# Performance work log

Measured on AMD Instinct MI355X. Metric: run time of the kernel, lower is better.

The kernel has to match this reference:

```python
import jax, jax.numpy as jnp
import numpy as np

B, M, N, DIM = 4, 3, 2048, 512
H = 4
HD = DIM // H  # 128
SCALE = float(np.sqrt(HD))  # code divides scores by sqrt(head_dim)


def setup_inputs() -> dict:
    key = jax.random.key(0)
    ks = jax.random.split(key, 9)
    s = 0.02
    return {
        "query": jax.random.normal(ks[0], (B, M, N, DIM), jnp.float32),
        "key": jax.random.normal(ks[1], (B, M, N, DIM), jnp.float32),
        "value": jax.random.normal(ks[2], (B, M, N, DIM), jnp.float32),
        "Wq": jax.random.normal(ks[3], (DIM, DIM), jnp.float32) * s,
        "bq": jax.random.normal(ks[4], (DIM,), jnp.float32) * s,
        "Wk": jax.random.normal(ks[5], (DIM, DIM), jnp.float32) * s,
        "bk": jax.random.normal(ks[6], (DIM,), jnp.float32) * s,
        "Wv": jax.random.normal(ks[7], (DIM, DIM), jnp.float32) * s,
        "bv": jax.random.normal(ks[8], (DIM,), jnp.float32) * s,
    }


def reference(query, key, value, Wq, bq, Wk, bk, Wv, bv):
    b, m, n, dim = query.shape
    # nn.Linear: x @ W.T + b
    Q = (query @ Wq.T + bq).reshape(b, m, n, H, HD)
    K = (key @ Wk.T + bk).reshape(b, m, n, H, HD)
    V = (value @ Wv.T + bv).reshape(b, m, n, H, HD)
    # scores: [b, m, H, n, n]
    scores = jnp.einsum("bmqhd,bmkhd->bmhqk", Q, K) / SCALE
    attn = jax.nn.softmax(scores, axis=-1)
    out = jnp.einsum("bmhqk,bmkhd->bmqhd", attn, V)
    return out.reshape(b, m, n, dim)
```

## Files before the change

kernel.cpp:

```cpp
#include <hip/hip_runtime.h>
#include <hip/hip_bf16.h>


typedef short s16x8 __attribute__((ext_vector_type(8)));
typedef unsigned short u16x8 __attribute__((ext_vector_type(8)));
typedef float f32x4 __attribute__((ext_vector_type(4)));

#define MFMA16(a, b, c) __builtin_amdgcn_mfma_f32_16x16x32_bf16((a), (b), (c), 0, 0, 0)

static __device__ __forceinline__ unsigned short f2bf(float f) {
    union { float f; unsigned u; } v; v.f = f;
    unsigned r = v.u + 0x7FFFu + ((v.u >> 16) & 1u);
    return (unsigned short)(r >> 16);
}
static __device__ __forceinline__ unsigned pk2(float a, float b) {
    unsigned r;
    asm("v_cvt_pk_bf16_f32 %0, %1, %2" : "=v"(r) : "v"(a), "v"(b));
    return r;
}
static __device__ __forceinline__ float exp2_hw(float x) {
    float r;
    asm("v_exp_f32 %0, %1" : "=v"(r) : "v"(x));
    return r;
}

#define CEXP_F 0.12755102905911087f

#define OSTR 72

__global__ __launch_bounds__(256, 2)
void qkv_proj_kernel(const float* __restrict__ Xq, const float* __restrict__ Xk,
                     const float* __restrict__ Xv,
                     const float* __restrict__ Wq, const float* __restrict__ bq,
                     const float* __restrict__ Wk, const float* __restrict__ bk,
                     const float* __restrict__ Wv, const float* __restrict__ bv,
                     unsigned short* __restrict__ ws_q,
                     unsigned short* __restrict__ ws_k,
                     unsigned short* __restrict__ ws_vt)
{
    __shared__ __align__(16) char smem[65536];

    const int which = blockIdx.z;
    const float* X    = (which == 0) ? Xq : (which == 1) ? Xk : Xv;
    const float* W    = (which == 0) ? Wq : (which == 1) ? Wk : Wv;
    const float* bias = (which == 0) ? bq : (which == 1) ? bk : bv;

    const int r0 = blockIdx.x * 128;
    const int c0 = blockIdx.y * 128;
    const int tid = threadIdx.x;
    const int lane = tid & 63, wave = tid >> 6;
    const int l15 = lane & 15, quad = lane >> 4;
    const int wr = (wave >> 1) * 64, wc = (wave & 1) * 64;

    const int srow = tid >> 4;
    const int scol = tid & 15;
    const int cf = scol * 4;
    const int cb = scol * 8;

    f32x4 acc[4][4] = {};

    {
        char* A0 = smem;
        char* B0 = smem + 16384;
        for (int i = 0; i < 8; ++i) {
            const int row = i * 16 + srow;
            float4 fa = *(const float4*)&X[(size_t)(r0 + row) * 512 + cf];
            float4 fb = *(const float4*)&W[(size_t)(c0 + row) * 512 + cf];
            uint2 wa, wb;
            wa.x = pk2(fa.x, fa.y); wa.y = pk2(fa.z, fa.w);
            wb.x = pk2(fb.x, fb.y); wb.y = pk2(fb.z, fb.w);
            const int sw = cb ^ ((row & 7) << 4);
            *(uint2*)(A0 + row * 128 + sw) = wa;
            *(uint2*)(B0 + row * 128 + sw) = wb;
        }
    }
    __syncthreads();

    for (int it = 0; it < 8; ++it) {
        char* Ac = smem + (it & 1) * 32768;
        char* Bc = Ac + 16384;
        const bool pre = (it < 7);

        float4 ra[8], rb[8];
        if (pre) {
            const int kn = (it + 1) * 64;
            for (int i = 0; i < 8; ++i) {
                const int row = i * 16 + srow;
                ra[i] = *(const float4*)&X[(size_t)(r0 + row) * 512 + kn + cf];
                rb[i] = *(const float4*)&W[(size_t)(c0 + row) * 512 + kn + cf];
            }
        }

        for (int kk = 0; kk < 2; ++kk) {
            s16x8 af[4], bf_[4];
            for (int mi = 0; mi < 4; ++mi) {
                const int row = wr + mi * 16 + l15;
                af[mi] = *(const s16x8*)(Ac + row * 128 +
                                         ((kk * 64 + quad * 16) ^ ((row & 7) << 4)));
            }
            for (int ni = 0; ni < 4; ++ni) {
                const int row = wc + ni * 16 + l15;
                bf_[ni] = *(const s16x8*)(Bc + row * 128 +
                                          ((kk * 64 + quad * 16) ^ ((row & 7) << 4)));
            }
            for (int mi = 0; mi < 4; ++mi)
                for (int ni = 0; ni < 4; ++ni)
                    acc[mi][ni] = MFMA16(af[mi], bf_[ni], acc[mi][ni]);
        }

        if (pre) {
            char* An = smem + ((it & 1) ^ 1) * 32768;
            char* Bn = An + 16384;
            for (int i = 0; i < 8; ++i) {
                const int row = i * 16 + srow;
                uint2 wa, wb;
                wa.x = pk2(ra[i].x, ra[i].y); wa.y = pk2(ra[i].z, ra[i].w);
                wb.x = pk2(rb[i].x, rb[i].y); wb.y = pk2(rb[i].z, rb[i].w);
                const int sw = cb ^ ((row & 7) << 4);
                *(uint2*)(An + row * 128 + sw) = wa;
                *(uint2*)(Bn + row * 128 + sw) = wb;
            }
        }
        __syncthreads();
    }

    float bvals[4];
    for (int ni = 0; ni < 4; ++ni) bvals[ni] = bias[c0 + wc + ni * 16 + l15];

    const float oscale = (which == 0) ? CEXP_F : 1.0f;

    __syncthreads();
    unsigned short* St = (unsigned short*)smem + wave * (64 * OSTR);
    const int h = blockIdx.y;
    const int bm = (r0 + wr) >> 11;
    const int n0 = (r0 + wr) & 2047;

    if (which != 2) {
        for (int mi = 0; mi < 4; ++mi)
            for (int ni = 0; ni < 4; ++ni)
                for (int r = 0; r < 4; ++r)
                    St[(mi * 16 + quad * 4 + r) * OSTR + ni * 16 + l15] =
                        f2bf((acc[mi][ni][r] + bvals[ni]) * oscale);
        unsigned short* dst = (which == 0) ? ws_q : ws_k;
        for (int p = 0; p < 8; ++p) {
            const int row = p * 8 + (lane >> 3);
            const int coff = (lane & 7) * 8;
            s16x8 v = *(const s16x8*)&St[row * OSTR + coff];
            *(s16x8*)&dst[((size_t)(bm * 4 + h) * 2048 + n0 + row) * 128 + wc + coff] = v;
        }
    } else {
        for (int mi = 0; mi < 4; ++mi)
            for (int ni = 0; ni < 4; ++ni)
                for (int r = 0; r < 4; ++r)
                    St[(ni * 16 + l15) * OSTR + mi * 16 + quad * 4 + r] =
                        f2bf(acc[mi][ni][r] + bvals[ni]);
        for (int p = 0; p < 8; ++p) {
            const int col = p * 8 + (lane >> 3);
            const int roff = (lane & 7) * 8;
            s16x8 v = *(const s16x8*)&St[col * OSTR + roff];
            *(s16x8*)&ws_vt[(((size_t)(bm * 4 + h)) * 128 + wc + col) * 2048 + n0 + roff] = v;
        }
    }
}

#define VSTR 80

__global__ __launch_bounds__(256)
void attn_kernel(const unsigned short* __restrict__ Qw,
                 const unsigned short* __restrict__ Kw,
                 const unsigned short* __restrict__ Vtw,
                 float* __restrict__ out)
{
    __shared__ char lds[36864];
    char* Kb0 = lds;
    char* Kb1 = lds + 8192;
    char* Vb0 = lds + 16384;
    char* Vb1 = lds + 26624;

    const int tid = threadIdx.x, lane = tid & 63, wave = tid >> 6;
    const int l15 = lane & 15, quad = lane >> 4;
    const int q0 = blockIdx.x * 128, h = blockIdx.y, bm = blockIdx.z;

    const unsigned short* Qh = Qw  + (size_t)(bm * 4 + h) * 2048 * 128;
    const unsigned short* Kh = Kw  + (size_t)(bm * 4 + h) * 2048 * 128;
    const unsigned short* Vh = Vtw + (size_t)(bm * 4 + h) * 128 * 2048;

    const int sk_key  = tid >> 3, sk_c   = tid & 7;
    const int sv_hd   = tid >> 1, sv_hlf = tid & 1;
    const int skx = sk_key & 7;
    const int krx = (l15 & 7) << 4;

    s16x8 qf[2][4];
    for (int qh = 0; qh < 2; ++qh)
        for (int kk = 0; kk < 4; ++kk)
            qf[qh][kk] = *(const s16x8*)&Qh[(size_t)(q0 + wave * 32 + qh * 16 + l15) * 128 + kk * 32 + quad * 8];

    s16x8 onesf;
    for (int i = 0; i < 8; ++i) onesf[i] = (short)0x3F80;

    {
        u16x8 ka = *(const u16x8*)&Kh[(size_t)sk_key * 128 + sk_c * 16];
        u16x8 kb = *(const u16x8*)&Kh[(size_t)sk_key * 128 + sk_c * 16 + 8];
        u16x8 va = *(const u16x8*)&Vh[(size_t)sv_hd * 2048 + sv_hlf * 16];
        u16x8 vb = *(const u16x8*)&Vh[(size_t)sv_hd * 2048 + sv_hlf * 16 + 8];
        *(u16x8*)(Kb0 + sk_key * 256 + (((sk_c * 2) ^ skx) << 4))     = ka;
        *(u16x8*)(Kb0 + sk_key * 256 + (((sk_c * 2 + 1) ^ skx) << 4)) = kb;
        *(u16x8*)(Vb0 + sv_hd * VSTR + sv_hlf * 32)      = va;
        *(u16x8*)(Vb0 + sv_hd * VSTR + sv_hlf * 32 + 16) = vb;
    }
    __syncthreads();

    f32x4 acc[2][8] = {};
    f32x4 accr[2] = {};

    for (int it = 0; it < 64; ++it) {
        const int k0 = it * 32;
        char* Kc = (it & 1) ? Kb1 : Kb0;
        char* Vc = (it & 1) ? Vb1 : Vb0;
        char* Kn = (it & 1) ? Kb0 : Kb1;
        char* Vn = (it & 1) ? Vb0 : Vb1;
        const bool do_stage = (it < 63);

        u16x8 ka, kb, va, vb;
        if (do_stage) {
            const int kn0 = k0 + 32;
            ka = *(const u16x8*)&Kh[(size_t)(kn0 + sk_key) * 128 + sk_c * 16];
            kb = *(const u16x8*)&Kh[(size_t)(kn0 + sk_key) * 128 + sk_c * 16 + 8];
            va = *(const u16x8*)&Vh[(size_t)sv_hd * 2048 + kn0 + sv_hlf * 16];
            vb = *(const u16x8*)&Vh[(size_t)sv_hd * 2048 + kn0 + sv_hlf * 16 + 8];
        }

        f32x4 s[2][2] = {};
        __builtin_amdgcn_s_setprio(1);
        for (int kk = 0; kk < 4; ++kk) {
            s16x8 kf0 = *(const s16x8*)(Kc + l15 * 256        + (((kk * 4 + quad) << 4) ^ krx));
            s16x8 kf1 = *(const s16x8*)(Kc + (16 + l15) * 256 + (((kk * 4 + quad) << 4) ^ krx));
            s[0][0] = MFMA16(kf0, qf[0][kk], s[0][0]);
            s[0][1] = MFMA16(kf1, qf[0][kk], s[0][1]);
            s[1][0] = MFMA16(kf0, qf[1][kk], s[1][0]);
            s[1][1] = MFMA16(kf1, qf[1][kk], s[1][1]);
        }
        __builtin_amdgcn_s_setprio(0);

        s16x8 pf[2];
        for (int qh = 0; qh < 2; ++qh) {
            const float p00 = exp2_hw(s[qh][0][0]);
            const float p01 = exp2_hw(s[qh][0][1]);
            const float p02 = exp2_hw(s[qh][0][2]);
            const float p03 = exp2_hw(s[qh][0][3]);
            const float p10 = exp2_hw(s[qh][1][0]);
            const float p11 = exp2_hw(s[qh][1][1]);
            const float p12 = exp2_hw(s[qh][1][2]);
            const float p13 = exp2_hw(s[qh][1][3]);
            unsigned x0 = pk2(p00, p01), y0 = pk2(p02, p03);
            unsigned x1 = pk2(p10, p11), y1 = pk2(p12, p13);
            asm("v_permlane32_swap_b32 %0, %1" : "+v"(x0), "+v"(x1));
            asm("v_permlane16_swap_b32 %0, %1" : "+v"(x0), "+v"(x1));
            asm("v_permlane32_swap_b32 %0, %1" : "+v"(y0), "+v"(y1));
            asm("v_permlane16_swap_b32 %0, %1" : "+v"(y0), "+v"(y1));
            union { unsigned u[4]; s16x8 v; } pu;
            pu.u[0] = x0; pu.u[1] = y0; pu.u[2] = x1; pu.u[3] = y1;
            pf[qh] = pu.v;
        }

        __builtin_amdgcn_s_setprio(1);
        accr[0] = MFMA16(onesf, pf[0], accr[0]);
        accr[1] = MFMA16(onesf, pf[1], accr[1]);
        for (int mb = 0; mb < 8; ++mb) {
            s16x8 vtf = *(const s16x8*)(Vc + (mb * 16 + l15) * VSTR + quad * 16);
            acc[0][mb] = MFMA16(vtf, pf[0], acc[0][mb]);
            acc[1][mb] = MFMA16(vtf, pf[1], acc[1][mb]);
        }
        __builtin_amdgcn_s_setprio(0);

        if (do_stage) {
            *(u16x8*)(Kn + sk_key * 256 + (((sk_c * 2) ^ skx) << 4))     = ka;
            *(u16x8*)(Kn + sk_key * 256 + (((sk_c * 2 + 1) ^ skx) << 4)) = kb;
            *(u16x8*)(Vn + sv_hd * VSTR + sv_hlf * 32)      = va;
            *(u16x8*)(Vn + sv_hd * VSTR + sv_hlf * 32 + 16) = vb;
        }

        __syncthreads();
    }

    for (int qh = 0; qh < 2; ++qh) {
        const float inv = 1.f / accr[qh][0];
        float* orow = out + ((size_t)bm * 2048 + q0 + wave * 32 + qh * 16 + l15) * 512 + h * 128;
        for (int mb = 0; mb < 8; ++mb) {
            float4 v;
            v.x = acc[qh][mb][0] * inv; v.y = acc[qh][mb][1] * inv;
            v.z = acc[qh][mb][2] * inv; v.w = acc[qh][mb][3] * inv;
            *(float4*)&orow[mb * 16 + quad * 4] = v;
        }
    }
}

extern "C" void kernel_launch(void* const* d_in, const int* in_sizes, int n_in,
                              void* d_out, int out_size, void* d_ws, size_t ws_size,
                              hipStream_t stream) {
    const float* Xq = (const float*)d_in[0];
    const float* Xk = (const float*)d_in[1];
    const float* Xv = (const float*)d_in[2];
    const float* Wq = (const float*)d_in[3];
    const float* bq = (const float*)d_in[4];
    const float* Wk = (const float*)d_in[5];
    const float* bk = (const float*)d_in[6];
    const float* Wv = (const float*)d_in[7];
    const float* bv = (const float*)d_in[8];
    float* out = (float*)d_out;

    unsigned short* ws = (unsigned short*)d_ws;
    const size_t per_tensor = (size_t)12 * 4 * 2048 * 128;
    unsigned short* ws_q  = ws;
    unsigned short* ws_k  = ws + per_tensor;
    unsigned short* ws_vt = ws + 2 * per_tensor;

    qkv_proj_kernel<<<dim3(192, 4, 3), 256, 0, stream>>>(
        Xq, Xk, Xv, Wq, bq, Wk, bk, Wv, bv, ws_q, ws_k, ws_vt);

    attn_kernel<<<dim3(16, 4, 12), 256, 0, stream>>>(ws_q, ws_k, ws_vt, out);
}
```

Baseline: 417.9 us.

## Stage QKV projection tiles via direct global-to-LDS loads, convert in registers

The QKV projection GEMM now copies fp32 X and W tiles straight into LDS with global_load_lds instead of loading into registers, converting to bf16 and storing. The bf16 conversion moves to the LDS read side, and the K step drops from 64 to 32 so 16 iterations keep the same 64 KB double buffer. The aim is to cut VGPR staging and let global loads overlap MFMA work asynchronously. In exchange, LDS traffic doubles (fp32 instead of bf16), and each element is converted once per wave that reads it rather than once in total.

```diff
diff --git a/kernel.cpp b/kernel.cpp
--- a/kernel.cpp
+++ b/kernel.cpp
@@ -5,6 +5,9 @@
 typedef short s16x8 __attribute__((ext_vector_type(8)));
 typedef unsigned short u16x8 __attribute__((ext_vector_type(8)));
 typedef float f32x4 __attribute__((ext_vector_type(4)));
+
+typedef const __attribute__((address_space(1))) void* gptr_t;
+typedef __attribute__((address_space(3))) void* lptr_t;
 
 #define MFMA16(a, b, c) __builtin_amdgcn_mfma_f32_16x16x32_bf16((a), (b), (c), 0, 0, 0)
 
@@ -52,77 +55,72 @@
     const int l15 = lane & 15, quad = lane >> 4;
     const int wr = (wave >> 1) * 64, wc = (wave & 1) * 64;
 
-    const int srow = tid >> 4;
-    const int scol = tid & 15;
-    const int cf = scol * 4;
-    const int cb = scol * 8;
+    const int g_row = lane >> 3;
+    const int g_gg  = (lane & 7) ^ (g_row & 7);
 
     f32x4 acc[4][4] = {};
 
-    {
-        char* A0 = smem;
-        char* B0 = smem + 16384;
-        for (int i = 0; i < 8; ++i) {
-            const int row = i * 16 + srow;
-            float4 fa = *(const float4*)&X[(size_t)(r0 + row) * 512 + cf];
-            float4 fb = *(const float4*)&W[(size_t)(c0 + row) * 512 + cf];
-            uint2 wa, wb;
-            wa.x = pk2(fa.x, fa.y); wa.y = pk2(fa.z, fa.w);
-            wb.x = pk2(fb.x, fb.y); wb.y = pk2(fb.z, fb.w);
-            const int sw = cb ^ ((row & 7) << 4);
-            *(uint2*)(A0 + row * 128 + sw) = wa;
-            *(uint2*)(B0 + row * 128 + sw) = wb;
-        }
-    }
+#define QKV_STAGE(BUF, IT) { \
+        const int k0_ = (IT) * 32; \
+        char* Ab_ = smem + (BUF) * 32768; \
+        char* Bb_ = Ab_ + 16384; \
+        _Pragma("unroll") \
+        for (int jj = 0; jj < 4; ++jj) { \
+            const int br_ = wave * 32 + jj * 8; \
+            const int row_ = br_ + g_row; \
+            const float* sa_ = &X[(size_t)(r0 + row_) * 512 + k0_ + g_gg * 4]; \
+            const float* sb_ = &W[(size_t)(c0 + row_) * 512 + k0_ + g_gg * 4]; \
+            __builtin_amdgcn_global_load_lds((gptr_t)(const void*)sa_, \
+                (lptr_t)(void*)(Ab_ + br_ * 128), 16, 0, 0); \
+            __builtin_amdgcn_global_load_lds((gptr_t)(const void*)sb_, \
+                (lptr_t)(void*)(Bb_ + br_ * 128), 16, 0, 0); \
+        } }
+
+#define QKV_MFMA(BUF) { \
+        char* Ac_ = smem + (BUF) * 32768; \
+        char* Bc_ = Ac_ + 16384; \
+        s16x8 af_[4], bf_[4]; \
+        _Pragma("unroll") \
+        for (int mi = 0; mi < 4; ++mi) { \
+            const int row_ = wr + mi * 16 + l15; \
+            const int x_ = row_ & 7; \
+            f32x4 lo_ = *(const f32x4*)(Ac_ + row_ * 128 + (((2 * quad) ^ x_) << 4)); \
+            f32x4 hi_ = *(const f32x4*)(Ac_ + row_ * 128 + (((2 * quad + 1) ^ x_) << 4)); \
+            union { unsigned u[4]; s16x8 v; } p_; \
+            p_.u[0] = pk2(lo_[0], lo_[1]); p_.u[1] = pk2(lo_[2], lo_[3]); \
+            p_.u[2] = pk2(hi_[0], hi_[1]); p_.u[3] = pk2(hi_[2], hi_[3]); \
+            af_[mi] = p_.v; \
+        } \
+        _Pragma("unroll") \
+        for (int ni = 0; ni < 4; ++ni) { \
+            const int row_ = wc + ni * 16 + l15; \
+            const int x_ = row_ & 7; \
+            f32x4 lo_ = *(const f32x4*)(Bc_ + row_ * 128 + (((2 * quad) ^ x_) << 4)); \
+            f32x4 hi_ = *(const f32x4*)(Bc_ + row_ * 128 + (((2 * quad + 1) ^ x_) << 4)); \
+            union { unsigned u[4]; s16x8 v; } p_; \
+            p_.u[0] = pk2(lo_[0], lo_[1]); p_.u[1] = pk2(lo_[2], lo_[3]); \
+            p_.u[2] = pk2(hi_[0], hi_[1]); p_.u[3] = pk2(hi_[2], hi_[3]); \
+            bf_[ni] = p_.v; \
+        } \
+        _Pragma("unroll") \
+        for (int mi = 0; mi < 4; ++mi) \
+            _Pragma("unroll") \
+            for (int ni = 0; ni < 4; ++ni) \
+                acc[mi][ni] = MFMA16(af_[mi], bf_[ni], acc[mi][ni]); \
+    }
+
+    QKV_STAGE(0, 0);
     __syncthreads();
 
-    for (int it = 0; it < 8; ++it) {
-        char* Ac = smem + (it & 1) * 32768;
-        char* Bc = Ac + 16384;
-        const bool pre = (it < 7);
-
-        float4 ra[8], rb[8];
-        if (pre) {
-            const int kn = (it + 1) * 64;
-            for (int i = 0; i < 8; ++i) {
-                const int row = i * 16 + srow;
-                ra[i] = *(const float4*)&X[(size_t)(r0 + row) * 512 + kn + cf];
-                rb[i] = *(const float4*)&W[(size_t)(c0 + row) * 512 + kn + cf];
-            }
-        }
-
-        for (int kk = 0; kk < 2; ++kk) {
-            s16x8 af[4], bf_[4];
-            for (int mi = 0; mi < 4; ++mi) {
-                const int row = wr + mi * 16 + l15;
-                af[mi] = *(const s16x8*)(Ac + row * 128 +
-                                         ((kk * 64 + quad * 16) ^ ((row & 7) << 4)));
-            }
-            for (int ni = 0; ni < 4; ++ni) {
-                const int row = wc + ni * 16 + l15;
-                bf_[ni] = *(const s16x8*)(Bc + row * 128 +
-                                          ((kk * 64 + quad * 16) ^ ((row & 7) << 4)));
-            }
-            for (int mi = 0; mi < 4; ++mi)
-                for (int ni = 0; ni < 4; ++ni)
-                    acc[mi][ni] = MFMA16(af[mi], bf_[ni], acc[mi][ni]);
-        }
-
-        if (pre) {
-            char* An = smem + ((it & 1) ^ 1) * 32768;
-            char* Bn = An + 16384;
-            for (int i = 0; i < 8; ++i) {
-                const int row = i * 16 + srow;
-                uint2 wa, wb;
-                wa.x = pk2(ra[i].x, ra[i].y); wa.y = pk2(ra[i].z, ra[i].w);
-                wb.x = pk2(rb[i].x, rb[i].y); wb.y = pk2(rb[i].z, rb[i].w);
-                const int sw = cb ^ ((row & 7) << 4);
-                *(uint2*)(An + row * 128 + sw) = wa;
-                *(uint2*)(Bn + row * 128 + sw) = wb;
-            }
-        }
+    for (int it = 0; it < 16; ++it) {
+        const int cur = it & 1;
+        if (it < 15) QKV_STAGE(cur ^ 1, it + 1);
+        QKV_MFMA(cur);
         __syncthreads();
     }
+
+#undef QKV_STAGE
+#undef QKV_MFMA
 
     float bvals[4];
     for (int ni = 0; ni < 4; ++ni) bvals[ni] = bias[c0 + wc + ni * 16 + l15];
```

New measurement: 385.3 us. 7.8% less time.
